# Kernel tuning notes

Hardware: AMD Instinct MI355X
Metric: run time of the kernel (lower is better)

The kernel has to match this reference:

```python
import jax, jax.numpy as jnp
import numpy as np

B = 65536
M = 16          # message_size
DEPTH = 6
WDL = 64
IN_DIM = 45 + 9 * M    # 9 mask + 4*9 board + 9*M messages
OUT_DIM = 9 * M


def setup_inputs() -> dict:
    key = jax.random.key(0)
    ks = jax.random.split(key, 8)
    input_mask = (jax.random.uniform(ks[0], (B, 9, 9)) < 0.5).astype(jnp.float32)
    input_board = (jax.random.uniform(ks[1], (B, 2, 10, 9)) < 0.5).astype(jnp.float32)
    # stacked per-om linears for every depth layer: [depth, 9, in, out]
    layer_w = jax.random.normal(ks[2], (DEPTH, 9, IN_DIM, OUT_DIM), jnp.float32) * (1.0 / np.sqrt(IN_DIM))
    layer_b = jnp.zeros((DEPTH, 9, OUT_DIM), jnp.float32)
    common_w = jax.random.normal(ks[3], (81 * M, 81 + WDL), jnp.float32) * (1.0 / np.sqrt(81 * M))
    common_b = jnp.zeros((81 + WDL,), jnp.float32)
    wdl_w = jax.random.normal(ks[4], (WDL, 3), jnp.float32) * (1.0 / np.sqrt(WDL))
    wdl_b = jnp.zeros((3,), jnp.float32)
    return {
        "input_mask": input_mask,
        "input_board": input_board,
        "layer_w": layer_w,
        "layer_b": layer_b,
        "common_w": common_w,
        "common_b": common_b,
        "wdl_w": wdl_w,
        "wdl_b": wdl_b,
    }


def reference(input_mask, input_board, layer_w, layer_b, common_w, common_b, wdl_w, wdl_b):
    b = input_mask.shape[0]
    m = layer_w.shape[-1] // 9
    depth = layer_w.shape[0]

    # per-om static features: mask[:,om], board[:,0,om], board[:,1,om], global cells
    g0 = jnp.broadcast_to(input_board[:, 0, 9:10, :], (b, 9, 9))
    g1 = jnp.broadcast_to(input_board[:, 1, 9:10, :], (b, 9, 9))
    static = jnp.concatenate(
        [input_mask, input_board[:, 0, :9, :], input_board[:, 1, :9, :], g0, g1],
        axis=-1,
    )  # [B, 9(om), 45]

    messages = jnp.zeros((b, 9, 9, m), input_mask.dtype)  # [B, src_om, dst_om, m]
    for d in range(depth):
        # messages[:, :, om, :] flattened -> gather along axis 2 for each om
        msg_in = messages.transpose(0, 2, 1, 3).reshape(b, 9, 9 * m)  # [B, om, 9m]
        x = jnp.concatenate([static, msg_in], axis=-1)  # [B, 9, 45+9m]
        # 9 distinct small linears, batched as one einsum
        h = jnp.einsum("boi,oij->boj", x, layer_w[d]) + layer_b[d]
        messages = jax.nn.relu(h).reshape(b, 9, 9, m)

    common = messages.reshape(b, 81 * m) @ common_w + common_b
    policy = common[:, :81]
    wdl_hidden = jax.nn.relu(common[:, 81:])
    wdl = wdl_hidden @ wdl_w + wdl_b
    return (wdl, policy)
```

## Files before the change

### kernel.cpp

```cpp
#include <hip/hip_runtime.h>
#include <hip/hip_bf16.h>
#include <stdint.h>


typedef __attribute__((ext_vector_type(4))) float    f32x4;
typedef __attribute__((ext_vector_type(4))) _Float16 f16x4;
typedef __attribute__((ext_vector_type(8))) _Float16 f16x8;
typedef unsigned long long u64;
typedef unsigned int u32;

#define STEP_BYTES 55296
#define PHA_SZ     30720
#define PHB_SZ     24576
#define CMN_STRIDE 41472
#define CSL_SZ     46080
#define CPA_SZ     23040
#define CPB_SZ     18432
#define WS_LAYER   (54*STEP_BYTES)
#define LDS_TOTAL  (2*PHA_SZ)

__device__ __forceinline__ unsigned short f2h(float f) {
  return __builtin_bit_cast(unsigned short, (_Float16)f);
}
__device__ __forceinline__ u64 as_u64(f16x4 v) { return __builtin_bit_cast(u64, v); }
__device__ __forceinline__ f16x4 as_f16x4(u64 v) { return __builtin_bit_cast(f16x4, v); }

__device__ __forceinline__ f32x4 mfma16(f16x4 a, f16x4 b, f32x4 c) {
#if __has_builtin(__builtin_amdgcn_mfma_f32_16x16x16f16)
  return __builtin_amdgcn_mfma_f32_16x16x16f16(a, b, c, 0, 0, 0);
#else
  asm("v_mfma_f32_16x16x16_f16 %0, %1, %2, %0" : "+v"(c) : "v"(a), "v"(b));
  return c;
#endif
}

__device__ __forceinline__ float static_feat(const float* __restrict__ mask,
                                             const float* __restrict__ board,
                                             int b, int o, int kidx) {
  if (kidx < 9)  return mask [b*81  + o*9 + kidx];
  if (kidx < 18) return board[b*180 +       o*9 + (kidx - 9)];
  if (kidx < 27) return board[b*180 + 90 +  o*9 + (kidx - 18)];
  if (kidx < 36) return board[b*180 +       81 + (kidx - 27)];
  if (kidx < 45) return board[b*180 + 90 +  81 + (kidx - 36)];
  return 0.f;
}

template<int NTH>
__device__ __forceinline__ void stage_n(const unsigned char* __restrict__ src,
                                        unsigned char* dstlds, int nbytes, int tid) {
  const int n16 = nbytes / 16;
  const int ubase = tid & ~63;
  for (int k = 0; k * NTH < n16; ++k) {
    const int idx = k * NTH + tid;
    if (idx < n16) {
      __builtin_amdgcn_global_load_lds(
          (const __attribute__((address_space(1))) void*)(src + (size_t)idx * 16),
          (__attribute__((address_space(3))) void*)(dstlds + (size_t)(k * NTH + ubase) * 16),
          16, 0, 0);
    }
  }
}


template<int P, int FIRST>
__device__ __forceinline__ void load_B(u64 (&B)[12],
    const unsigned char* __restrict__ stat, const unsigned char* __restrict__ msg,
    int o, int b0, int s15, int hq, int Bt)
{
  const size_t lo = (size_t)(b0 + s15) * 32 + (size_t)hq * 8;
  B[0] = *(const u64*)(stat + ((size_t)(o * 2 + 0) * Bt) * 32 + lo);
  B[1] = *(const u64*)(stat + ((size_t)(o * 2 + 1) * Bt) * 32 + lo);
  B[2] = *(const u64*)(stat + ((size_t)18 * Bt) * 32 + lo);
  if (!FIRST) {
#pragma unroll
    for (int i = 0; i < 9; ++i) {
      const int cell = P ? (o * 9 + i) : (i * 9 + o);
      B[3 + i] = *(const u64*)(msg + ((size_t)cell * Bt) * 32 + lo);
    }
  }
}

template<int P, int FIRST>
__global__ __launch_bounds__(512, 4) void layer_step(
    const unsigned char* __restrict__ wsLW, const unsigned char* __restrict__ stat,
    unsigned char* __restrict__ msg, int d, int Bt)
{
  __shared__ unsigned char panel[STEP_BYTES];
  const int tid = threadIdx.x;
  const int lane = tid & 63;
  const int wid = tid >> 6;
  const int o = blockIdx.y;
  const int s15 = lane & 15, hq = lane >> 4;

  stage_n<512>(wsLW + (size_t)(d * 9 + o) * STEP_BYTES, panel, STEP_BYTES, tid);

  const int b0 = blockIdx.x * 256 + wid * 32;
  u64 B0[12], B1[12];
  load_B<P, FIRST>(B0, stat, msg, o, b0,      s15, hq, Bt);
  load_B<P, FIRST>(B1, stat, msg, o, b0 + 16, s15, hq, Bt);

  asm volatile("s_waitcnt vmcnt(0)" ::: "memory");
  __syncthreads();

  const unsigned char* pl = panel + (size_t)lane * 16;
  const size_t lo0 = (size_t)(b0 + s15) * 32 + (size_t)hq * 8;
  const size_t lo1 = lo0 + 16 * 32;
#pragma unroll
  for (int j = 0; j < 9; ++j) {
    f32x4 a0 = 0.f, a1 = 0.f;
#pragma unroll
    for (int s = 0; s < (FIRST ? 2 : 6); ++s) {
      const f16x8 af = *(const f16x8*)(pl + j * 6144 + s * 1024);
      const f16x4 alo = __builtin_shufflevector(af, af, 0, 1, 2, 3);
      a0 = mfma16(alo, as_f16x4(B0[2 * s]), a0);
      a1 = mfma16(alo, as_f16x4(B1[2 * s]), a1);
      if (!FIRST || s == 0) {
        const f16x4 ahi = __builtin_shufflevector(af, af, 4, 5, 6, 7);
        a0 = mfma16(ahi, as_f16x4(B0[2 * s + 1]), a0);
        a1 = mfma16(ahi, as_f16x4(B1[2 * s + 1]), a1);
      }
    }
    f16x4 h0, h1;
#pragma unroll
    for (int r = 0; r < 4; ++r) {
      h0[r] = (_Float16)fmaxf(a0[r], 0.f);
      h1[r] = (_Float16)fmaxf(a1[r], 0.f);
    }
    const int wcell = P ? (o * 9 + j) : (j * 9 + o);
    unsigned char* wp = msg + ((size_t)wcell * Bt) * 32;
    *(u64*)(wp + lo0) = as_u64(h0);
    *(u64*)(wp + lo1) = as_u64(h1);
  }
}

__global__ __launch_bounds__(256, 3) void common_unf(
    const unsigned char* __restrict__ wsCW, const unsigned char* __restrict__ msg,
    const float* __restrict__ common_b, const float* __restrict__ wdl_w,
    const float* __restrict__ wdl_b, float* __restrict__ out, int Bt)
{
  __shared__ unsigned char sl[CSL_SZ];
  const int tid = threadIdx.x;
  const int lane = tid & 63;
  const int wid = tid >> 6;
  const int s15 = lane & 15, hq = lane >> 4;
  const int b0 = blockIdx.x * 128 + wid * 32;
  const size_t lo0 = (size_t)(b0 + s15) * 32 + (size_t)hq * 8;
  const size_t lo1 = lo0 + 16 * 32;

  f32x4 acc0[10], acc1[10];
#pragma unroll
  for (int mt = 0; mt < 10; ++mt) { acc0[mt] = 0.f; acc1[mt] = 0.f; }

  for (int i = 0; i < 9; ++i) {
    __syncthreads();
    stage_n<256>(wsCW + (size_t)i * CSL_SZ, sl, CSL_SZ, tid);

    u64 m0[9], m1[9];
#pragma unroll
    for (int jj = 0; jj < 9; ++jj) {
      const unsigned char* mp = msg + ((size_t)(i * 9 + jj) * Bt) * 32;
      m0[jj] = *(const u64*)(mp + lo0);
      m1[jj] = *(const u64*)(mp + lo1);
    }
    asm volatile("s_waitcnt vmcnt(0)" ::: "memory");
    __syncthreads();

#pragma unroll
    for (int mt = 0; mt < 10; ++mt) {
      const unsigned char* base = sl + mt * 4608;
#pragma unroll
      for (int p = 0; p < 4; ++p) {
        const f16x8 a8 = *(const f16x8*)(base + p * 1024 + (size_t)lane * 16);
        const f16x4 alo = __builtin_shufflevector(a8, a8, 0, 1, 2, 3);
        const f16x4 ahi = __builtin_shufflevector(a8, a8, 4, 5, 6, 7);
        acc0[mt] = mfma16(alo, as_f16x4(m0[2 * p]),     acc0[mt]);
        acc1[mt] = mfma16(alo, as_f16x4(m1[2 * p]),     acc1[mt]);
        acc0[mt] = mfma16(ahi, as_f16x4(m0[2 * p + 1]), acc0[mt]);
        acc1[mt] = mfma16(ahi, as_f16x4(m1[2 * p + 1]), acc1[mt]);
      }
      const f16x4 al = *(const f16x4*)(base + 4096 + (size_t)lane * 8);
      acc0[mt] = mfma16(al, as_f16x4(m0[8]), acc0[mt]);
      acc1[mt] = mfma16(al, as_f16x4(m1[8]), acc1[mt]);
    }
  }

  float pw0[3] = {0.f, 0.f, 0.f}, pw1[3] = {0.f, 0.f, 0.f};
#pragma unroll
  for (int mt = 0; mt < 10; ++mt) {
#pragma unroll
    for (int r = 0; r < 4; ++r) {
      const int c = mt * 16 + 4 * hq + r;
      if (c < 81) {
        out[(size_t)3 * Bt + (size_t)(b0 + s15) * 81 + c]      = acc0[mt][r] + common_b[c];
        out[(size_t)3 * Bt + (size_t)(b0 + 16 + s15) * 81 + c] = acc1[mt][r] + common_b[c];
      } else if (c < 145) {
        const float h0 = fmaxf(acc0[mt][r] + common_b[c], 0.f);
        const float h1 = fmaxf(acc1[mt][r] + common_b[c], 0.f);
        const int cc = c - 81;
#pragma unroll
        for (int w = 0; w < 3; ++w) {
          const float wv = wdl_w[cc * 3 + w];
          pw0[w] += h0 * wv;
          pw1[w] += h1 * wv;
        }
      }
    }
  }
#pragma unroll
  for (int w = 0; w < 3; ++w) {
    float v0 = pw0[w], v1 = pw1[w];
    v0 += __shfl_xor(v0, 16, 64); v0 += __shfl_xor(v0, 32, 64);
    v1 += __shfl_xor(v1, 16, 64); v1 += __shfl_xor(v1, 32, 64);
    if (hq == 0) {
      const float bb = wdl_b[w];
      out[(size_t)(b0 + s15) * 3 + w]      = v0 + bb;
      out[(size_t)(b0 + 16 + s15) * 3 + w] = v1 + bb;
    }
  }
}

__global__ __launch_bounds__(256) void conv_static(
    const float* __restrict__ mask, const float* __restrict__ board,
    unsigned char* __restrict__ stat, int Bt)
{
  __shared__ float sm[16 * 81];
  __shared__ float sb[16 * 180];
  const int tid = threadIdx.x;
  const int base_b = blockIdx.x * 16;

  const float4* gm = (const float4*)(mask + (size_t)base_b * 81);
  for (int idx = tid; idx < 324; idx += 256) ((float4*)sm)[idx] = gm[idx];
  const float4* gb = (const float4*)(board + (size_t)base_b * 180);
  for (int idx = tid; idx < 720; idx += 256) ((float4*)sb)[idx] = gb[idx];
  __syncthreads();

  const int lane = tid & 63, wv = tid >> 6;
  const int s15 = lane & 15, hq = lane >> 4;
  const float* lm = sm + s15 * 81;
  const float* lb = sb + s15 * 180;
  for (int slot = wv; slot < 19; slot += 4) {
    const int o = (slot < 18) ? (slot >> 1) : 0;
    const int c = (slot < 18) ? (slot & 1) : 2;
    unsigned short v[4];
#pragma unroll
    for (int e = 0; e < 4; ++e) {
      const int kidx = c * 16 + 4 * hq + e;
      float f;
      if (kidx < 9)        f = lm[o * 9 + kidx];
      else if (kidx < 18)  f = lb[o * 9 + (kidx - 9)];
      else if (kidx < 27)  f = lb[90 + o * 9 + (kidx - 18)];
      else if (kidx < 36)  f = lb[81 + (kidx - 27)];
      else if (kidx < 45)  f = lb[90 + 81 + (kidx - 36)];
      else                 f = (kidx == 45) ? 1.f : 0.f;
      v[e] = f2h(f);
    }
    const u32 w0 = (u32)v[0] | ((u32)v[1] << 16);
    const u32 w1 = (u32)v[2] | ((u32)v[3] << 16);
    *(uint2*)(stat + ((size_t)slot * Bt + base_b + s15) * 32 + (size_t)hq * 8)
        = make_uint2(w0, w1);
  }
}

__global__ __launch_bounds__(256) void conv_common_w2(const float* __restrict__ cw,
                                                      unsigned char* __restrict__ dst) {
  const int gid = blockIdx.x * 256 + threadIdx.x;
  const int NPAIR = 10 * 36 * 64;
  if (gid < NPAIR) {
    const int lane = gid & 63;
    const int t = gid >> 6;
    const int p = t % 4, t2 = t / 4;
    const int i = t2 % 9, mt = t2 / 9;
    const int m = lane & 15, hq = lane >> 4;
    const int c = mt * 16 + m;
    unsigned short v[8];
#pragma unroll
    for (int e = 0; e < 8; ++e) {
      const int ci = i * 9 + 2 * p + (e >> 2);
      const int k = ci * 16 + 4 * hq + (e & 3);
      v[e] = f2h((c < 145) ? cw[(size_t)k * 145 + c] : 0.f);
    }
    const u32 w0 = (u32)v[0] | ((u32)v[1] << 16);
    const u32 w1 = (u32)v[2] | ((u32)v[3] << 16);
    const u32 w2 = (u32)v[4] | ((u32)v[5] << 16);
    const u32 w3 = (u32)v[6] | ((u32)v[7] << 16);
    *(uint4*)(dst + (size_t)i * CSL_SZ + (size_t)mt * 4608
              + (size_t)p * 1024 + (size_t)lane * 16) = make_uint4(w0, w1, w2, w3);
  } else if (gid < NPAIR + 10 * 9 * 64) {
    const int g = gid - NPAIR;
    const int lane = g & 63;
    const int t = g >> 6;
    const int i = t % 9, mt = t / 9;
    const int m = lane & 15, hq = lane >> 4;
    const int c = mt * 16 + m;
    unsigned short v[4];
#pragma unroll
    for (int e = 0; e < 4; ++e) {
      const int k = (i * 9 + 8) * 16 + 4 * hq + e;
      v[e] = f2h((c < 145) ? cw[(size_t)k * 145 + c] : 0.f);
    }
    const u32 w0 = (u32)v[0] | ((u32)v[1] << 16);
    const u32 w1 = (u32)v[2] | ((u32)v[3] << 16);
    *(uint2*)(dst + (size_t)i * CSL_SZ + (size_t)mt * 4608
              + 4096 + (size_t)lane * 8) = make_uint2(w0, w1);
  }
}


template<int P, int O, int J0, int J1, int OFF>
__device__ __forceinline__ void jt_range(const unsigned char* __restrict__ buf,
    u64 (&msg)[9][9], const u64 (&msgc)[9], f16x4 st0, f16x4 st1, f16x4 stc, int lane)
{
  const unsigned char* abase = buf + (size_t)lane * 16 - OFF;
#pragma unroll
  for (int j = J0; j < J1; ++j) {
    f32x4 acc = 0.f;
#pragma unroll
    for (int sp = 0; sp < 6; ++sp) {
      const f16x8 af = *(const f16x8*)(abase + j * 6144 + sp * 1024);
      const f16x4 alo = __builtin_shufflevector(af, af, 0, 1, 2, 3);
      const f16x4 ahi = __builtin_shufflevector(af, af, 4, 5, 6, 7);
      const int c0 = 2 * sp, c1 = 2 * sp + 1;
      if (c0 == 0)      acc = mfma16(alo, st0, acc);
      else if (c0 == 2) acc = mfma16(alo, stc, acc);
      else              acc = mfma16(alo, as_f16x4(msgc[c0 - 3]), acc);
      if (c1 == 1)      acc = mfma16(ahi, st1, acc);
      else              acc = mfma16(ahi, as_f16x4(msgc[c1 - 3]), acc);
    }
    f16x4 h;
#pragma unroll
    for (int r = 0; r < 4; ++r)
      h[r] = (_Float16)fmaxf(acc[r], 0.f);
    if (P) msg[O][j] = as_u64(h); else msg[j][O] = as_u64(h);
  }
}

template<int P, int O>
__device__ __forceinline__ void do_step_layer(int base, const unsigned char* __restrict__ ws,
    unsigned char* bufA, unsigned char* bufB, u64 (&msg)[9][9],
    u64 sb, u32 sb8, f16x4 stc, int lane, int tid)
{
  const int step = base + P * 9 + O;
  asm volatile("s_waitcnt vmcnt(0)" ::: "memory");
  __syncthreads();
  stage_n<256>(ws + (size_t)step * STEP_BYTES + PHA_SZ, bufB, PHB_SZ, tid);
  f16x4 st0, st1;
  {
    const u32 byt = (O < 8) ? ((u32)(sb >> (O * 8)) & 0xFFu) : sb8;
#pragma unroll
    for (int e = 0; e < 4; ++e) {
      st0[e] = (_Float16)(float)((byt >> e) & 1u);
      st1[e] = (_Float16)(float)((byt >> (4 + e)) & 1u);
    }
  }
  u64 msgc[9];
#pragma unroll
  for (int i = 0; i < 9; ++i)
    msgc[i] = P ? msg[O][i] : msg[i][O];
  jt_range<P, O, 0, 5, 0>(bufA, msg, msgc, st0, st1, stc, lane);
  asm volatile("s_waitcnt vmcnt(0)" ::: "memory");
  __syncthreads();
  if (step + 1 < 54)
    stage_n<256>(ws + (size_t)(step + 1) * STEP_BYTES, bufA, PHA_SZ, tid);
  else
    stage_n<256>(ws + WS_LAYER, bufA, CPA_SZ, tid);
  jt_range<P, O, 5, 9, PHA_SZ>(bufB, msg, msgc, st0, st1, stc, lane);
}

__global__ __launch_bounds__(256, 1) void mix_main(
    const float* __restrict__ mask, const float* __restrict__ board,
    const float* __restrict__ common_b, const float* __restrict__ wdl_w,
    const float* __restrict__ wdl_b, const unsigned char* __restrict__ ws,
    float* __restrict__ out, int Bt)
{
  extern __shared__ unsigned char lds[];
  const int tid = threadIdx.x;
  const int lane = tid & 63;
  const int wid = tid >> 6;
  const int s15 = lane & 15, hq = lane >> 4;
  const int b0 = blockIdx.x * 64 + wid * 16;
  unsigned char* bufA = lds;
  unsigned char* bufB = lds + PHA_SZ;

  stage_n<256>(ws, bufA, PHA_SZ, tid);

  u64 msg[9][9];
#pragma unroll
  for (int a = 0; a < 9; ++a)
#pragma unroll
    for (int b = 0; b < 9; ++b) msg[a][b] = 0ull;

  u64 sb = 0ull;
  u32 sb8 = 0u;
  {
    const int b = b0 + s15;
#pragma unroll
    for (int o = 0; o < 9; ++o)
#pragma unroll
      for (int e = 0; e < 4; ++e) {
        const u32 bit0 = static_feat(mask, board, b, o,      4 * hq + e) > 0.5f;
        const u32 bit1 = static_feat(mask, board, b, o, 16 + 4 * hq + e) > 0.5f;
        if (o < 8) sb |= ((u64)bit0 << (o * 8 + e)) | ((u64)bit1 << (o * 8 + 4 + e));
        else       sb8 |= (bit0 << e) | (bit1 << (4 + e));
      }
  }
  f16x4 stc;
  {
    const int b = b0 + s15;
#pragma unroll
    for (int e = 0; e < 4; ++e) {
      const int kidx = 32 + 4 * hq + e;
      stc[e] = (_Float16)((kidx == 45) ? 1.f : static_feat(mask, board, b, 0, kidx));
    }
  }

#define DO_POS(P, O) do_step_layer<P, O>(base, ws, bufA, bufB, msg, sb, sb8, stc, lane, tid);
  for (int dp = 0; dp < 3; ++dp) {
    const int base = dp * 18;
    DO_POS(0,0) DO_POS(0,1) DO_POS(0,2) DO_POS(0,3) DO_POS(0,4)
    DO_POS(0,5) DO_POS(0,6) DO_POS(0,7) DO_POS(0,8)
    DO_POS(1,0) DO_POS(1,1) DO_POS(1,2) DO_POS(1,3) DO_POS(1,4)
    DO_POS(1,5) DO_POS(1,6) DO_POS(1,7) DO_POS(1,8)
  }
#undef DO_POS

  float pw[3] = {0.f, 0.f, 0.f};
  for (int mt = 0; mt < 10; ++mt) {
    asm volatile("s_waitcnt vmcnt(0)" ::: "memory");
    __syncthreads();
    stage_n<256>(ws + WS_LAYER + (size_t)mt * CMN_STRIDE + CPA_SZ, bufB, CPB_SZ, tid);
    f32x4 a0 = 0.f;
#pragma unroll
    for (int i = 0; i < 5; ++i) {
      const unsigned char* base = bufA + i * 4608;
#pragma unroll
      for (int p = 0; p < 4; ++p) {
        const f16x8 af = *(const f16x8*)(base + p * 1024 + (size_t)lane * 16);
        const f16x4 alo = __builtin_shufflevector(af, af, 0, 1, 2, 3);
        const f16x4 ahi = __builtin_shufflevector(af, af, 4, 5, 6, 7);
        a0 = mfma16(alo, as_f16x4(msg[i][2 * p]),     a0);
        a0 = mfma16(ahi, as_f16x4(msg[i][2 * p + 1]), a0);
      }
      const f16x4 al = *(const f16x4*)(bufA + i * 4608 + 4096 + (size_t)lane * 8);
      a0 = mfma16(al, as_f16x4(msg[i][8]), a0);
    }
    asm volatile("s_waitcnt vmcnt(0)" ::: "memory");
    __syncthreads();
    if (mt + 1 < 10)
      stage_n<256>(ws + WS_LAYER + (size_t)(mt + 1) * CMN_STRIDE, bufA, CPA_SZ, tid);
#pragma unroll
    for (int i = 5; i < 9; ++i) {
      const unsigned char* base = bufB + i * 4608 - CPA_SZ;
#pragma unroll
      for (int p = 0; p < 4; ++p) {
        const f16x8 af = *(const f16x8*)(base + p * 1024 + (size_t)lane * 16);
        const f16x4 alo = __builtin_shufflevector(af, af, 0, 1, 2, 3);
        const f16x4 ahi = __builtin_shufflevector(af, af, 4, 5, 6, 7);
        a0 = mfma16(alo, as_f16x4(msg[i][2 * p]),     a0);
        a0 = mfma16(ahi, as_f16x4(msg[i][2 * p + 1]), a0);
      }
      const f16x4 al = *(const f16x4*)(base + 4096 + (size_t)lane * 8);
      a0 = mfma16(al, as_f16x4(msg[i][8]), a0);
    }
#pragma unroll
    for (int r = 0; r < 4; ++r) {
      const int c = mt * 16 + 4 * hq + r;
      const float bias = (c < 145) ? common_b[c] : 0.f;
      const float v0 = a0[r] + bias;
      if (c < 81) {
        out[(size_t)3 * Bt + (size_t)(b0 + s15) * 81 + c] = v0;
      } else if (c < 145) {
        const float h0 = fmaxf(v0, 0.f);
        const int cc = c - 81;
#pragma unroll
        for (int w = 0; w < 3; ++w)
          pw[w] += h0 * wdl_w[cc * 3 + w];
      }
    }
  }
#pragma unroll
  for (int w = 0; w < 3; ++w) {
    float v0 = pw[w];
    v0 += __shfl_xor(v0, 16, 64); v0 += __shfl_xor(v0, 32, 64);
    if (hq == 0)
      out[(size_t)(b0 + s15) * 3 + w] = v0 + wdl_b[w];
  }
}


__global__ __launch_bounds__(256) void conv_layer_w(const float* __restrict__ lw,
                                                    const float* __restrict__ lb,
                                                    unsigned char* __restrict__ dst) {
  const int gid = blockIdx.x * 256 + threadIdx.x;
  if (gid >= 54 * 9 * 6 * 64) return;
  const int lane = gid & 63;
  const int t = gid >> 6;
  const int kp = t % 6, t2 = t / 6;
  const int jp = t2 % 9, dop = t2 / 9;
  const int m = lane & 15, hq = lane >> 4;
  unsigned short v[8];
#pragma unroll
  for (int e = 0; e < 8; ++e) {
    const int kc = kp * 2 + (e >> 2);
    const int kidx = kc * 16 + 4 * hq + (e & 3);
    float f = 0.f;
    if (kidx < 45)        f = lw[((size_t)dop * 189 + kidx) * 144 + jp * 16 + m];
    else if (kidx == 45)  f = lb[(size_t)dop * 144 + jp * 16 + m];
    else if (kidx >= 48)  f = lw[((size_t)dop * 189 + (kidx - 3)) * 144 + jp * 16 + m];
    v[e] = f2h(f);
  }
  const u32 w0 = (u32)v[0] | ((u32)v[1] << 16);
  const u32 w1 = (u32)v[2] | ((u32)v[3] << 16);
  const u32 w2 = (u32)v[4] | ((u32)v[5] << 16);
  const u32 w3 = (u32)v[6] | ((u32)v[7] << 16);
  *(uint4*)(dst + (size_t)gid * 16) = make_uint4(w0, w1, w2, w3);
}

__global__ __launch_bounds__(256) void conv_common_w(const float* __restrict__ cw,
                                                     unsigned char* __restrict__ dst) {
  const int gid = blockIdx.x * 256 + threadIdx.x;
  const int NPAIR = 10 * 36 * 64;
  if (gid < NPAIR) {
    const int lane = gid & 63;
    const int t = gid >> 6;
    const int p = t % 4, t2 = t / 4;
    const int i = t2 % 9, mt = t2 / 9;
    const int m = lane & 15, hq = lane >> 4;
    const int c = mt * 16 + m;
    unsigned short v[8];
#pragma unroll
    for (int e = 0; e < 8; ++e) {
      const int ci = i * 9 + 2 * p + (e >> 2);
      const int k = ci * 16 + 4 * hq + (e & 3);
      v[e] = f2h((c < 145) ? cw[(size_t)k * 145 + c] : 0.f);
    }
    const u32 w0 = (u32)v[0] | ((u32)v[1] << 16);
    const u32 w1 = (u32)v[2] | ((u32)v[3] << 16);
    const u32 w2 = (u32)v[4] | ((u32)v[5] << 16);
    const u32 w3 = (u32)v[6] | ((u32)v[7] << 16);
    *(uint4*)(dst + (size_t)WS_LAYER + (size_t)mt * CMN_STRIDE + (size_t)i * 4608
              + (size_t)p * 1024 + (size_t)lane * 16) = make_uint4(w0, w1, w2, w3);
  } else if (gid < NPAIR + 10 * 9 * 64) {
    const int g = gid - NPAIR;
    const int lane = g & 63;
    const int t = g >> 6;
    const int i = t % 9, mt = t / 9;
    const int m = lane & 15, hq = lane >> 4;
    const int c = mt * 16 + m;
    unsigned short v[4];
#pragma unroll
    for (int e = 0; e < 4; ++e) {
      const int k = (i * 9 + 8) * 16 + 4 * hq + e;
      v[e] = f2h((c < 145) ? cw[(size_t)k * 145 + c] : 0.f);
    }
    const u32 w0 = (u32)v[0] | ((u32)v[1] << 16);
    const u32 w1 = (u32)v[2] | ((u32)v[3] << 16);
    *(uint2*)(dst + (size_t)WS_LAYER + (size_t)mt * CMN_STRIDE + (size_t)i * 4608
              + 4096 + (size_t)lane * 8) = make_uint2(w0, w1);
  }
}


extern "C" void kernel_launch(void* const* d_in, const int* in_sizes, int n_in,
                              void* d_out, int out_size, void* d_ws, size_t ws_size,
                              hipStream_t stream) {
  const float* mask     = (const float*)d_in[0];
  const float* board    = (const float*)d_in[1];
  const float* layer_w  = (const float*)d_in[2];
  const float* layer_b  = (const float*)d_in[3];
  const float* common_w = (const float*)d_in[4];
  const float* common_b = (const float*)d_in[5];
  const float* wdl_w    = (const float*)d_in[6];
  const float* wdl_b    = (const float*)d_in[7];
  float* out = (float*)d_out;
  unsigned char* ws = (unsigned char*)d_ws;
  const int Bt = in_sizes[0] / 81;

  const size_t WS_CW_OFF   = (size_t)WS_LAYER;
  const size_t WS_STAT_OFF = WS_CW_OFF + (size_t)9 * CSL_SZ;
  const size_t WS_MSG_OFF  = WS_STAT_OFF + (size_t)19 * Bt * 32;
  const size_t WS_NEED     = WS_MSG_OFF + (size_t)81 * Bt * 32;

  hipLaunchKernelGGL(conv_layer_w, dim3((54 * 9 * 6 * 64) / 256), dim3(256), 0, stream,
                     layer_w, layer_b, ws);

  if (ws_size >= WS_NEED) {
    unsigned char* stat = ws + WS_STAT_OFF;
    unsigned char* msgp = ws + WS_MSG_OFF;

    hipLaunchKernelGGL(conv_common_w2, dim3((10 * (36 + 9) * 64 + 255) / 256), dim3(256),
                       0, stream, common_w, ws + WS_CW_OFF);
    hipLaunchKernelGGL(conv_static, dim3(Bt / 16), dim3(256), 0, stream,
                       mask, board, stat, Bt);

    const dim3 lgrid(Bt / 256, 9);
    hipLaunchKernelGGL((layer_step<0, 1>), lgrid, dim3(512), 0, stream, ws, stat, msgp, 0, Bt);
    hipLaunchKernelGGL((layer_step<1, 0>), lgrid, dim3(512), 0, stream, ws, stat, msgp, 1, Bt);
    hipLaunchKernelGGL((layer_step<0, 0>), lgrid, dim3(512), 0, stream, ws, stat, msgp, 2, Bt);
    hipLaunchKernelGGL((layer_step<1, 0>), lgrid, dim3(512), 0, stream, ws, stat, msgp, 3, Bt);
    hipLaunchKernelGGL((layer_step<0, 0>), lgrid, dim3(512), 0, stream, ws, stat, msgp, 4, Bt);
    hipLaunchKernelGGL((layer_step<1, 0>), lgrid, dim3(512), 0, stream, ws, stat, msgp, 5, Bt);

    hipLaunchKernelGGL(common_unf, dim3(Bt / 128), dim3(256), 0, stream,
                       ws + WS_CW_OFF, msgp, common_b, wdl_w, wdl_b, out, Bt);
  } else {
    hipLaunchKernelGGL(conv_common_w, dim3((10 * (36 + 9) * 64 + 255) / 256), dim3(256),
                       0, stream, common_w, ws);
    (void)hipFuncSetAttribute((const void*)mix_main,
                              hipFuncAttributeMaxDynamicSharedMemorySize, LDS_TOTAL);
    hipLaunchKernelGGL(mix_main, dim3(Bt / 64), dim3(256), LDS_TOTAL, stream,
                       mask, board, common_b, wdl_w, wdl_b, ws, out, Bt);
  }
}
```

Before: 451.7 us.

## Process batch in chunks so message buffers stay cache-resident across layers

Splits the batch into chunks of 32768 and runs all six layer steps plus the common head per chunk, using a batch offset argument. The aim is to keep each chunk's fp16 message working set in the last-level cache between layer kernels instead of streaming the full batch through HBM. In exchange the number of kernel launches doubles and each launch has half the blocks, which lowers parallelism per launch. The fast path now also requires the batch size to be a multiple of the chunk size.

```diff
diff --git a/kernel.cpp b/kernel.cpp
--- a/kernel.cpp
+++ b/kernel.cpp
@@ -18,6 +18,7 @@
 #define CPB_SZ     18432
 #define WS_LAYER   (54*STEP_BYTES)
 #define LDS_TOTAL  (2*PHA_SZ)
+#define CHUNK      32768
 
 __device__ __forceinline__ unsigned short f2h(float f) {
   return __builtin_bit_cast(unsigned short, (_Float16)f);
@@ -83,7 +84,7 @@
 template<int P, int FIRST>
 __global__ __launch_bounds__(512, 4) void layer_step(
     const unsigned char* __restrict__ wsLW, const unsigned char* __restrict__ stat,
-    unsigned char* __restrict__ msg, int d, int Bt)
+    unsigned char* __restrict__ msg, int d, int Bt, int boff)
 {
   __shared__ unsigned char panel[STEP_BYTES];
   const int tid = threadIdx.x;
@@ -94,7 +95,7 @@
 
   stage_n<512>(wsLW + (size_t)(d * 9 + o) * STEP_BYTES, panel, STEP_BYTES, tid);
 
-  const int b0 = blockIdx.x * 256 + wid * 32;
+  const int b0 = boff + blockIdx.x * 256 + wid * 32;
   u64 B0[12], B1[12];
   load_B<P, FIRST>(B0, stat, msg, o, b0,      s15, hq, Bt);
   load_B<P, FIRST>(B1, stat, msg, o, b0 + 16, s15, hq, Bt);
@@ -136,14 +137,14 @@
 __global__ __launch_bounds__(256, 3) void common_unf(
     const unsigned char* __restrict__ wsCW, const unsigned char* __restrict__ msg,
     const float* __restrict__ common_b, const float* __restrict__ wdl_w,
-    const float* __restrict__ wdl_b, float* __restrict__ out, int Bt)
+    const float* __restrict__ wdl_b, float* __restrict__ out, int Bt, int boff)
 {
   __shared__ unsigned char sl[CSL_SZ];
   const int tid = threadIdx.x;
   const int lane = tid & 63;
   const int wid = tid >> 6;
   const int s15 = lane & 15, hq = lane >> 4;
-  const int b0 = blockIdx.x * 128 + wid * 32;
+  const int b0 = boff + blockIdx.x * 128 + wid * 32;
   const size_t lo0 = (size_t)(b0 + s15) * 32 + (size_t)hq * 8;
   const size_t lo1 = lo0 + 16 * 32;
 
@@ -583,7 +584,7 @@
   hipLaunchKernelGGL(conv_layer_w, dim3((54 * 9 * 6 * 64) / 256), dim3(256), 0, stream,
                      layer_w, layer_b, ws);
 
-  if (ws_size >= WS_NEED) {
+  if (ws_size >= WS_NEED && Bt % CHUNK == 0) {
     unsigned char* stat = ws + WS_STAT_OFF;
     unsigned char* msgp = ws + WS_MSG_OFF;
 
@@ -592,16 +593,17 @@
     hipLaunchKernelGGL(conv_static, dim3(Bt / 16), dim3(256), 0, stream,
                        mask, board, stat, Bt);
 
-    const dim3 lgrid(Bt / 256, 9);
-    hipLaunchKernelGGL((layer_step<0, 1>), lgrid, dim3(512), 0, stream, ws, stat, msgp, 0, Bt);
-    hipLaunchKernelGGL((layer_step<1, 0>), lgrid, dim3(512), 0, stream, ws, stat, msgp, 1, Bt);
-    hipLaunchKernelGGL((layer_step<0, 0>), lgrid, dim3(512), 0, stream, ws, stat, msgp, 2, Bt);
-    hipLaunchKernelGGL((layer_step<1, 0>), lgrid, dim3(512), 0, stream, ws, stat, msgp, 3, Bt);
-    hipLaunchKernelGGL((layer_step<0, 0>), lgrid, dim3(512), 0, stream, ws, stat, msgp, 4, Bt);
-    hipLaunchKernelGGL((layer_step<1, 0>), lgrid, dim3(512), 0, stream, ws, stat, msgp, 5, Bt);
-
-    hipLaunchKernelGGL(common_unf, dim3(Bt / 128), dim3(256), 0, stream,
-                       ws + WS_CW_OFF, msgp, common_b, wdl_w, wdl_b, out, Bt);
+    const dim3 lgrid(CHUNK / 256, 9);
+    for (int boff = 0; boff < Bt; boff += CHUNK) {
+      hipLaunchKernelGGL((layer_step<0, 1>), lgrid, dim3(512), 0, stream, ws, stat, msgp, 0, Bt, boff);
+      hipLaunchKernelGGL((layer_step<1, 0>), lgrid, dim3(512), 0, stream, ws, stat, msgp, 1, Bt, boff);
+      hipLaunchKernelGGL((layer_step<0, 0>), lgrid, dim3(512), 0, stream, ws, stat, msgp, 2, Bt, boff);
+      hipLaunchKernelGGL((layer_step<1, 0>), lgrid, dim3(512), 0, stream, ws, stat, msgp, 3, Bt, boff);
+      hipLaunchKernelGGL((layer_step<0, 0>), lgrid, dim3(512), 0, stream, ws, stat, msgp, 4, Bt, boff);
+      hipLaunchKernelGGL((layer_step<1, 0>), lgrid, dim3(512), 0, stream, ws, stat, msgp, 5, Bt, boff);
+      hipLaunchKernelGGL(common_unf, dim3(CHUNK / 128), dim3(256), 0, stream,
+                         ws + WS_CW_OFF, msgp, common_b, wdl_w, wdl_b, out, Bt, boff);
+    }
   } else {
     hipLaunchKernelGGL(conv_common_w, dim3((10 * (36 + 9) * 64 + 255) / 256), dim3(256),
                        0, stream, common_w, ws);
```

Result: slower. 477.3 us (+5.7%).
